# Kernel tuning notes

Measured on AMD Instinct MI355X. Metric: run time of the kernel, lower is better.

Reference implementation:

```python
import jax, jax.numpy as jnp
import numpy as np

N = 8192
D_IN = 1024
D_OUT = 1024


def setup_inputs() -> dict:
    key = jax.random.key(0)
    k0, k1, k2, k3 = jax.random.split(key, 4)
    scale = 1.0 / np.sqrt(D_IN)  # roughly matches nn.Linear init magnitude
    return {
        "x": jax.random.normal(k0, (N, D_IN), dtype=jnp.float32),
        "Wq": jax.random.normal(k1, (D_IN, D_OUT), dtype=jnp.float32) * scale,
        "Wk": jax.random.normal(k2, (D_IN, D_OUT), dtype=jnp.float32) * scale,
        "Wv": jax.random.normal(k3, (D_IN, D_OUT), dtype=jnp.float32) * scale,
    }


def reference(x, Wq, Wk, Wv):
    # QKV projections (bias-free Linear); weights stored [d_in, d_out]
    q = x @ Wq  # [N, d_out]
    k = x @ Wk  # [N, d_out]
    v = x @ Wv  # [N, d_out]
    # full N x N attention scores, scaled by sqrt(d_out), softmax over keys
    scores = jnp.einsum("nd,md->nm", q, k) / jnp.sqrt(jnp.asarray(k.shape[-1], x.dtype))
    weights = jax.nn.softmax(scores, axis=-1)
    return weights @ v  # [N, d_out]
```

## Files before the change

### kernel.cpp

```cpp
#include <hip/hip_runtime.h>
#include <hip/hip_bf16.h>
#include <stdint.h>
#include <stddef.h>

using bf16 = __hip_bfloat16;

typedef __attribute__((ext_vector_type(8))) short bf16x8;
typedef __attribute__((ext_vector_type(4))) float f32x4;

#define NROWS 8192
#define DDIM  1024

#define GLDS16(gsrc, ldst)                                                     \
  __builtin_amdgcn_global_load_lds(                                            \
      (const __attribute__((address_space(1))) uint32_t*)(gsrc),               \
      (__attribute__((address_space(3))) uint32_t*)(ldst), 16, 0, 0)

__global__ void cvt_f32_bf16_k(const float* __restrict__ in, bf16* __restrict__ out, int n) {
  int i = blockIdx.x * blockDim.x + threadIdx.x;
  int idx = i * 4;
  if (idx < n) {
    float4 v = *reinterpret_cast<const float4*>(in + idx);
    alignas(8) bf16 t[4] = {(bf16)v.x, (bf16)v.y, (bf16)v.z, (bf16)v.w};
    *reinterpret_cast<uint2*>(out + idx) = *reinterpret_cast<const uint2*>(t);
  }
}

template <typename Tin>
__global__ void transpose_bf16_k(const Tin* __restrict__ in, bf16* __restrict__ out,
                                 int R, int C) {
  __shared__ float tile[32][33];
  int bx = blockIdx.x * 32;
  int by = blockIdx.y * 32;
  int tx = threadIdx.x, ty = threadIdx.y;
#pragma unroll
  for (int i = 0; i < 32; i += 8)
    tile[ty + i][tx] = (float)in[(size_t)(by + ty + i) * C + (bx + tx)];
  __syncthreads();
#pragma unroll
  for (int i = 0; i < 32; i += 8)
    out[(size_t)(bx + ty + i) * R + (by + tx)] = (bf16)tile[tx][ty + i];
}

__global__ void rowsum_k(const bf16* __restrict__ P, float* __restrict__ Z, int Kc) {
  int lane = threadIdx.x & 63;
  int wave = threadIdx.x >> 6;
  int row = blockIdx.x * 4 + wave;
  const bf16* p = P + (size_t)row * Kc;
  float s = 0.f;
  for (int c = lane * 8; c < Kc; c += 64 * 8) {
    bf16x8 v = *reinterpret_cast<const bf16x8*>(p + c);
#pragma unroll
    for (int j = 0; j < 8; j++)
      s += __uint_as_float(((uint32_t)(uint16_t)v[j]) << 16);
  }
#pragma unroll
  for (int off = 32; off > 0; off >>= 1) s += __shfl_down(s, off);
  if (lane == 0) Z[row] = s;
}

__global__ void combine_k(const float* __restrict__ P0, const float* __restrict__ P1,
                          const float* __restrict__ Z, float* __restrict__ out, int total) {
  int i = blockIdx.x * blockDim.x + threadIdx.x;
  int idx = i * 4;
  if (idx < total) {
    float4 a = *reinterpret_cast<const float4*>(P0 + idx);
    float4 b = *reinterpret_cast<const float4*>(P1 + idx);
    float rz = 1.0f / Z[idx >> 10];
    float4 o;
    o.x = (a.x + b.x) * rz; o.y = (a.y + b.y) * rz;
    o.z = (a.z + b.z) * rz; o.w = (a.w + b.w) * rz;
    *reinterpret_cast<float4*>(out + idx) = o;
  }
}

template <int EPI>
__global__ __launch_bounds__(256) void gemm_bt_k(
    const bf16* __restrict__ A, const bf16* __restrict__ B, void* __restrict__ Cv,
    const float* __restrict__ Z, int M, int N, int K, float scale) {
  __shared__ alignas(16) bf16 As[128 * 32];
  __shared__ alignas(16) bf16 Bs[128 * 32];

  const int tid = threadIdx.x;
  const int lane = tid & 63;
  const int wave = tid >> 6;
  const int wr = (wave >> 1) * 64;
  const int wc = (wave & 1) * 64;

  const int mBase = blockIdx.y * 128;
  const int nBase = blockIdx.x * 128;

  const int srow = tid >> 2;
  const int skel = (tid & 3) * 8;

  const bf16* gA0 = A + (size_t)(mBase + srow) * K + skel;
  const bf16* gA1 = A + (size_t)(mBase + srow + 64) * K + skel;
  const bf16* gB0 = B + (size_t)(nBase + srow) * K + skel;
  const bf16* gB1 = B + (size_t)(nBase + srow + 64) * K + skel;

  bf16* lA0 = &As[srow * 32 + skel];
  bf16* lA1 = &As[(srow + 64) * 32 + skel];
  bf16* lB0 = &Bs[srow * 32 + skel];
  bf16* lB1 = &Bs[(srow + 64) * 32 + skel];

  f32x4 acc[4][4];
  f32x4 zero = {0.f, 0.f, 0.f, 0.f};
#pragma unroll
  for (int i = 0; i < 4; i++)
#pragma unroll
    for (int j = 0; j < 4; j++) acc[i][j] = zero;

  const int fr = lane & 15;
  const int fk = (lane >> 4) * 8;

  for (int k0 = 0; k0 < K; k0 += 32) {
    GLDS16(gA0 + k0, lA0);
    GLDS16(gA1 + k0, lA1);
    GLDS16(gB0 + k0, lB0);
    GLDS16(gB1 + k0, lB1);
    __syncthreads();

    bf16x8 a[4], b[4];
#pragma unroll
    for (int mi = 0; mi < 4; mi++)
      a[mi] = *reinterpret_cast<const bf16x8*>(&As[(wr + mi * 16 + fr) * 32 + fk]);
#pragma unroll
    for (int nj = 0; nj < 4; nj++)
      b[nj] = *reinterpret_cast<const bf16x8*>(&Bs[(wc + nj * 16 + fr) * 32 + fk]);
#pragma unroll
    for (int mi = 0; mi < 4; mi++)
#pragma unroll
      for (int nj = 0; nj < 4; nj++)
        acc[mi][nj] = __builtin_amdgcn_mfma_f32_16x16x32_bf16(a[mi], b[nj], acc[mi][nj], 0, 0, 0);
    __syncthreads();
  }

#pragma unroll
  for (int mi = 0; mi < 4; mi++) {
#pragma unroll
    for (int nj = 0; nj < 4; nj++) {
      int col = nBase + wc + nj * 16 + fr;
#pragma unroll
      for (int j = 0; j < 4; j++) {
        int row = mBase + wr + mi * 16 + (lane >> 4) * 4 + j;
        float v = acc[mi][nj][j];
        if (EPI == 0) {
          ((bf16*)Cv)[(size_t)row * N + col] = (bf16)(v * scale);
        }
      }
    }
  }
}

template <int EPI>
__global__ __launch_bounds__(512, 2) void gemm256_k(
    const bf16* __restrict__ A, const bf16* __restrict__ B, void* __restrict__ Cv,
    int M, int N, int K, int ksplit) {
  __shared__ alignas(1024) bf16 smem[4 * 16384];

  const int tid = threadIdx.x;
  const int lane = tid & 63;
  const int wave = tid >> 6;
  const int wm = wave >> 2;
  const int wn = wave & 3;

  const int nwgx = gridDim.x;
  const int nwg = nwgx * gridDim.y;
  const int wg = blockIdx.y * nwgx + blockIdx.x;
  const int cpx = nwg >> 3;
  const int swz = (wg & 7) * cpx + (wg >> 3);
  const int bx = swz % nwgx;
  const int by = swz / nwgx;
  const int mBase = by * 256;
  const int nBase = bx * 256;

  const int z = blockIdx.z;
  const int kbase = z * ksplit;
  const int NT = ksplit / 32;

  const int sr = lane >> 2;
  const int ssl = (lane & 3) ^ ((lane >> 3) & 3);
  const bf16* srcA0 = A + (size_t)(mBase + wave * 16 + sr) * K + kbase + ssl * 8;
  const bf16* srcA1 = A + (size_t)(mBase + (wave + 8) * 16 + sr) * K + kbase + ssl * 8;
  const bf16* srcB0 = B + (size_t)(nBase + wave * 16 + sr) * K + kbase + ssl * 8;
  const bf16* srcB1 = B + (size_t)(nBase + (wave + 8) * 16 + sr) * K + kbase + ssl * 8;

  const int fr = lane & 15;
  const int laneElem = fr * 32 + (((lane >> 4) ^ ((fr >> 1) & 3)) * 8);

  f32x4 acc[8][4];
  f32x4 zero = {0.f, 0.f, 0.f, 0.f};
#pragma unroll
  for (int m = 0; m < 8; m++)
#pragma unroll
    for (int n = 0; n < 4; n++) acc[m][n] = zero;

  auto stage = [&](int t) {
    bf16* base = smem + (t & 3) * 16384;
    int kk = t * 32;
    GLDS16(srcA0 + kk, base + wave * 512);
    GLDS16(srcA1 + kk, base + (wave + 8) * 512);
    GLDS16(srcB0 + kk, base + 8192 + wave * 512);
    GLDS16(srcB1 + kk, base + 8192 + (wave + 8) * 512);
  };

  stage(0);
  if (NT > 1) stage(1);
  if (NT > 2) stage(2);

  for (int t = 0; t < NT; ++t) {
    __builtin_amdgcn_s_barrier();
    if (t + 3 < NT) stage(t + 3);
    int infl = NT - 1 - t;
    if (infl > 3) infl = 3;
    if (infl == 3)      asm volatile("s_waitcnt vmcnt(12)" ::: "memory");
    else if (infl == 2) asm volatile("s_waitcnt vmcnt(8)" ::: "memory");
    else if (infl == 1) asm volatile("s_waitcnt vmcnt(4)" ::: "memory");
    else                asm volatile("s_waitcnt vmcnt(0)" ::: "memory");
    __builtin_amdgcn_s_barrier();

    const bf16* bufA = smem + (t & 3) * 16384;
    const bf16* bufB = bufA + 8192;
    bf16x8 a[8], b[4];
#pragma unroll
    for (int m = 0; m < 8; m++)
      a[m] = *reinterpret_cast<const bf16x8*>(bufA + (wm * 128 + m * 16) * 32 + laneElem);
#pragma unroll
    for (int n = 0; n < 4; n++)
      b[n] = *reinterpret_cast<const bf16x8*>(bufB + (wn * 64 + n * 16) * 32 + laneElem);
#pragma unroll
    for (int m = 0; m < 8; m++)
#pragma unroll
      for (int n = 0; n < 4; n++)
        acc[m][n] = __builtin_amdgcn_mfma_f32_16x16x32_bf16(a[m], b[n], acc[m][n], 0, 0, 0);
  }

#pragma unroll
  for (int m = 0; m < 8; m++) {
#pragma unroll
    for (int n = 0; n < 4; n++) {
      int col = nBase + wn * 64 + n * 16 + fr;
#pragma unroll
      for (int j = 0; j < 4; j++) {
        int row = mBase + wm * 128 + m * 16 + (lane >> 4) * 4 + j;
        float v = acc[m][n][j];
        if (EPI == 1) {
          ((bf16*)Cv)[(size_t)row * N + col] = (bf16)__expf(v);
        } else {
          float* Cp = (float*)Cv + (size_t)z * M * N;
          Cp[(size_t)row * N + col] = v;
        }
      }
    }
  }
}

extern "C" void kernel_launch(void* const* d_in, const int* in_sizes, int n_in,
                              void* d_out, int out_size, void* d_ws, size_t ws_size,
                              hipStream_t stream) {
  (void)in_sizes; (void)n_in; (void)out_size; (void)ws_size;
  const float* x  = (const float*)d_in[0];
  const float* Wq = (const float*)d_in[1];
  const float* Wk = (const float*)d_in[2];
  const float* Wv = (const float*)d_in[3];
  float* out = (float*)d_out;

  char* ws = (char*)d_ws;
  const size_t MB = 1024 * 1024;
  size_t o = 0;
  float* Z  = (float*)(ws + o); o += 64 * 1024;
  size_t xb_off = o;
  bf16* xb  = (bf16*)(ws + o); o += (size_t)NROWS * DDIM * 2;
  bf16* WqT = (bf16*)(ws + o); o += (size_t)DDIM * DDIM * 2;
  bf16* WkT = (bf16*)(ws + o); o += (size_t)DDIM * DDIM * 2;
  bf16* WvT = (bf16*)(ws + o); o += (size_t)DDIM * DDIM * 2;
  bf16* Qb  = (bf16*)(ws + o); o += (size_t)NROWS * DDIM * 2;
  bf16* Kb  = (bf16*)(ws + o); o += (size_t)NROWS * DDIM * 2;
  bf16* Vb  = (bf16*)(ws + o); o += (size_t)NROWS * DDIM * 2;
  bf16* Vt  = (bf16*)(ws + o); o += (size_t)DDIM * NROWS * 2;
  bf16* P   = (bf16*)(ws + o); o += (size_t)NROWS * NROWS * 2;
  float* Pp = (float*)(ws + xb_off);
  (void)MB;

  {
    int n = NROWS * DDIM;
    cvt_f32_bf16_k<<<(n / 4 + 255) / 256, 256, 0, stream>>>(x, xb, n);
  }
  {
    dim3 tb(32, 8);
    transpose_bf16_k<float><<<dim3(32, 32), tb, 0, stream>>>(Wq, WqT, DDIM, DDIM);
    transpose_bf16_k<float><<<dim3(32, 32), tb, 0, stream>>>(Wk, WkT, DDIM, DDIM);
    transpose_bf16_k<float><<<dim3(32, 32), tb, 0, stream>>>(Wv, WvT, DDIM, DDIM);
  }
  {
    dim3 grid(DDIM / 128, NROWS / 128);
    gemm_bt_k<0><<<grid, 256, 0, stream>>>(xb, WqT, Qb, nullptr, NROWS, DDIM, DDIM, 0.03125f);
    gemm_bt_k<0><<<grid, 256, 0, stream>>>(xb, WkT, Kb, nullptr, NROWS, DDIM, DDIM, 1.0f);
    gemm_bt_k<0><<<grid, 256, 0, stream>>>(xb, WvT, Vb, nullptr, NROWS, DDIM, DDIM, 1.0f);
  }
  {
    dim3 tb(32, 8);
    transpose_bf16_k<bf16><<<dim3(DDIM / 32, NROWS / 32), tb, 0, stream>>>(Vb, Vt, NROWS, DDIM);
  }
  gemm256_k<1><<<dim3(NROWS / 256, NROWS / 256, 1), 512, 0, stream>>>(
      Qb, Kb, P, NROWS, NROWS, DDIM, DDIM);
  rowsum_k<<<NROWS / 4, 256, 0, stream>>>(P, Z, NROWS);
  gemm256_k<3><<<dim3(DDIM / 256, NROWS / 256, 2), 512, 0, stream>>>(
      P, Vt, Pp, NROWS, DDIM, NROWS, NROWS / 2);
  {
    int total = NROWS * DDIM;
    combine_k<<<(total / 4 + 255) / 256, 256, 0, stream>>>(
        Pp, Pp + (size_t)NROWS * DDIM, Z, out, total);
  }
}
```

Measured before the change: 435.3 us.

## Fuse QKV projections, fuse rowsum into exp epilogue, double-buffer LDS fragment reads

Merges the three projection GEMMs into one wide GEMM on the 256-tile kernel, writing an interleaved QKV buffer with stride-aware loads. The softmax row sums are now accumulated in the exp epilogue using shuffles and atomics, so the separate rowsum pass over P is dropped. The main loop is unrolled by two and prefetches the next tile's LDS fragments into registers while MFMAs run, with setprio hints. The trade-offs are atomic contention on Z, higher register pressure, and a memset added to the launch sequence.

```diff
diff --git a/kernel.cpp b/kernel.cpp
--- a/kernel.cpp
+++ b/kernel.cpp
@@ -28,35 +28,18 @@
 
 template <typename Tin>
 __global__ void transpose_bf16_k(const Tin* __restrict__ in, bf16* __restrict__ out,
-                                 int R, int C) {
+                                 int R, int C, int ldin) {
   __shared__ float tile[32][33];
   int bx = blockIdx.x * 32;
   int by = blockIdx.y * 32;
   int tx = threadIdx.x, ty = threadIdx.y;
 #pragma unroll
   for (int i = 0; i < 32; i += 8)
-    tile[ty + i][tx] = (float)in[(size_t)(by + ty + i) * C + (bx + tx)];
+    tile[ty + i][tx] = (float)in[(size_t)(by + ty + i) * ldin + (bx + tx)];
   __syncthreads();
 #pragma unroll
   for (int i = 0; i < 32; i += 8)
     out[(size_t)(bx + ty + i) * R + (by + tx)] = (bf16)tile[tx][ty + i];
-}
-
-__global__ void rowsum_k(const bf16* __restrict__ P, float* __restrict__ Z, int Kc) {
-  int lane = threadIdx.x & 63;
-  int wave = threadIdx.x >> 6;
-  int row = blockIdx.x * 4 + wave;
-  const bf16* p = P + (size_t)row * Kc;
-  float s = 0.f;
-  for (int c = lane * 8; c < Kc; c += 64 * 8) {
-    bf16x8 v = *reinterpret_cast<const bf16x8*>(p + c);
-#pragma unroll
-    for (int j = 0; j < 8; j++)
-      s += __uint_as_float(((uint32_t)(uint16_t)v[j]) << 16);
-  }
-#pragma unroll
-  for (int off = 32; off > 0; off >>= 1) s += __shfl_down(s, off);
-  if (lane == 0) Z[row] = s;
 }
 
 __global__ void combine_k(const float* __restrict__ P0, const float* __restrict__ P1,
@@ -75,87 +58,10 @@
 }
 
 template <int EPI>
-__global__ __launch_bounds__(256) void gemm_bt_k(
-    const bf16* __restrict__ A, const bf16* __restrict__ B, void* __restrict__ Cv,
-    const float* __restrict__ Z, int M, int N, int K, float scale) {
-  __shared__ alignas(16) bf16 As[128 * 32];
-  __shared__ alignas(16) bf16 Bs[128 * 32];
-
-  const int tid = threadIdx.x;
-  const int lane = tid & 63;
-  const int wave = tid >> 6;
-  const int wr = (wave >> 1) * 64;
-  const int wc = (wave & 1) * 64;
-
-  const int mBase = blockIdx.y * 128;
-  const int nBase = blockIdx.x * 128;
-
-  const int srow = tid >> 2;
-  const int skel = (tid & 3) * 8;
-
-  const bf16* gA0 = A + (size_t)(mBase + srow) * K + skel;
-  const bf16* gA1 = A + (size_t)(mBase + srow + 64) * K + skel;
-  const bf16* gB0 = B + (size_t)(nBase + srow) * K + skel;
-  const bf16* gB1 = B + (size_t)(nBase + srow + 64) * K + skel;
-
-  bf16* lA0 = &As[srow * 32 + skel];
-  bf16* lA1 = &As[(srow + 64) * 32 + skel];
-  bf16* lB0 = &Bs[srow * 32 + skel];
-  bf16* lB1 = &Bs[(srow + 64) * 32 + skel];
-
-  f32x4 acc[4][4];
-  f32x4 zero = {0.f, 0.f, 0.f, 0.f};
-#pragma unroll
-  for (int i = 0; i < 4; i++)
-#pragma unroll
-    for (int j = 0; j < 4; j++) acc[i][j] = zero;
-
-  const int fr = lane & 15;
-  const int fk = (lane >> 4) * 8;
-
-  for (int k0 = 0; k0 < K; k0 += 32) {
-    GLDS16(gA0 + k0, lA0);
-    GLDS16(gA1 + k0, lA1);
-    GLDS16(gB0 + k0, lB0);
-    GLDS16(gB1 + k0, lB1);
-    __syncthreads();
-
-    bf16x8 a[4], b[4];
-#pragma unroll
-    for (int mi = 0; mi < 4; mi++)
-      a[mi] = *reinterpret_cast<const bf16x8*>(&As[(wr + mi * 16 + fr) * 32 + fk]);
-#pragma unroll
-    for (int nj = 0; nj < 4; nj++)
-      b[nj] = *reinterpret_cast<const bf16x8*>(&Bs[(wc + nj * 16 + fr) * 32 + fk]);
-#pragma unroll
-    for (int mi = 0; mi < 4; mi++)
-#pragma unroll
-      for (int nj = 0; nj < 4; nj++)
-        acc[mi][nj] = __builtin_amdgcn_mfma_f32_16x16x32_bf16(a[mi], b[nj], acc[mi][nj], 0, 0, 0);
-    __syncthreads();
-  }
-
-#pragma unroll
-  for (int mi = 0; mi < 4; mi++) {
-#pragma unroll
-    for (int nj = 0; nj < 4; nj++) {
-      int col = nBase + wc + nj * 16 + fr;
-#pragma unroll
-      for (int j = 0; j < 4; j++) {
-        int row = mBase + wr + mi * 16 + (lane >> 4) * 4 + j;
-        float v = acc[mi][nj][j];
-        if (EPI == 0) {
-          ((bf16*)Cv)[(size_t)row * N + col] = (bf16)(v * scale);
-        }
-      }
-    }
-  }
-}
-
-template <int EPI>
 __global__ __launch_bounds__(512, 2) void gemm256_k(
     const bf16* __restrict__ A, const bf16* __restrict__ B, void* __restrict__ Cv,
-    int M, int N, int K, int ksplit) {
+    float* __restrict__ Zp, int M, int N, int K, int lda, int ldb, int ldc,
+    int ksplit, float scale) {
   __shared__ alignas(1024) bf16 smem[4 * 16384];
 
   const int tid = threadIdx.x;
@@ -180,10 +86,10 @@
 
   const int sr = lane >> 2;
   const int ssl = (lane & 3) ^ ((lane >> 3) & 3);
-  const bf16* srcA0 = A + (size_t)(mBase + wave * 16 + sr) * K + kbase + ssl * 8;
-  const bf16* srcA1 = A + (size_t)(mBase + (wave + 8) * 16 + sr) * K + kbase + ssl * 8;
-  const bf16* srcB0 = B + (size_t)(nBase + wave * 16 + sr) * K + kbase + ssl * 8;
-  const bf16* srcB1 = B + (size_t)(nBase + (wave + 8) * 16 + sr) * K + kbase + ssl * 8;
+  const bf16* srcA0 = A + (size_t)(mBase + wave * 16 + sr) * lda + kbase + ssl * 8;
+  const bf16* srcA1 = A + (size_t)(mBase + (wave + 8) * 16 + sr) * lda + kbase + ssl * 8;
+  const bf16* srcB0 = B + (size_t)(nBase + wave * 16 + sr) * ldb + kbase + ssl * 8;
+  const bf16* srcB1 = B + (size_t)(nBase + (wave + 8) * 16 + sr) * ldb + kbase + ssl * 8;
 
   const int fr = lane & 15;
   const int laneElem = fr * 32 + (((lane >> 4) ^ ((fr >> 1) & 3)) * 8);
@@ -203,36 +109,80 @@
     GLDS16(srcB0 + kk, base + 8192 + wave * 512);
     GLDS16(srcB1 + kk, base + 8192 + (wave + 8) * 512);
   };
+  auto rdA = [&](const bf16* buf, int m) {
+    return *reinterpret_cast<const bf16x8*>(buf + wm * 4096 + m * 512 + laneElem);
+  };
+  auto rdB = [&](const bf16* buf, int n) {
+    return *reinterpret_cast<const bf16x8*>(buf + 8192 + wn * 2048 + n * 512 + laneElem);
+  };
+
+  bf16x8 fA0[8], fB0[4], fA1[8], fB1[4];
+
+  auto compute = [&](int t, bf16x8 (&aC)[8], bf16x8 (&bC)[4],
+                     bf16x8 (&aN)[8], bf16x8 (&bN)[4], bool rd) {
+    const bf16* nb = smem + ((t + 1) & 3) * 16384;
+#pragma unroll
+    for (int c = 0; c < 4; c++) {
+      if (rd) {
+        aN[2 * c]     = rdA(nb, 2 * c);
+        aN[2 * c + 1] = rdA(nb, 2 * c + 1);
+        bN[c]         = rdB(nb, c);
+      }
+      __builtin_amdgcn_s_setprio(1);
+#pragma unroll
+      for (int mm = 0; mm < 2; mm++)
+#pragma unroll
+        for (int n = 0; n < 4; n++)
+          acc[2 * c + mm][n] = __builtin_amdgcn_mfma_f32_16x16x32_bf16(
+              aC[2 * c + mm], bC[n], acc[2 * c + mm][n], 0, 0, 0);
+      __builtin_amdgcn_s_setprio(0);
+    }
+  };
 
   stage(0);
-  if (NT > 1) stage(1);
-  if (NT > 2) stage(2);
-
-  for (int t = 0; t < NT; ++t) {
-    __builtin_amdgcn_s_barrier();
-    if (t + 3 < NT) stage(t + 3);
-    int infl = NT - 1 - t;
-    if (infl > 3) infl = 3;
-    if (infl == 3)      asm volatile("s_waitcnt vmcnt(12)" ::: "memory");
-    else if (infl == 2) asm volatile("s_waitcnt vmcnt(8)" ::: "memory");
-    else if (infl == 1) asm volatile("s_waitcnt vmcnt(4)" ::: "memory");
-    else                asm volatile("s_waitcnt vmcnt(0)" ::: "memory");
-    __builtin_amdgcn_s_barrier();
-
-    const bf16* bufA = smem + (t & 3) * 16384;
-    const bf16* bufB = bufA + 8192;
-    bf16x8 a[8], b[4];
+  stage(1);
+  stage(2);
+  asm volatile("s_waitcnt vmcnt(8)" ::: "memory");
+  __builtin_amdgcn_s_barrier();
+#pragma unroll
+  for (int m = 0; m < 8; m++) fA0[m] = rdA(smem, m);
+#pragma unroll
+  for (int n = 0; n < 4; n++) fB0[n] = rdB(smem, n);
+
+#define WAITV(infl)                                                            \
+  do {                                                                         \
+    if ((infl) >= 2)      asm volatile("s_waitcnt vmcnt(8)" ::: "memory");     \
+    else if ((infl) == 1) asm volatile("s_waitcnt vmcnt(4)" ::: "memory");     \
+    else                  asm volatile("s_waitcnt vmcnt(0)" ::: "memory");     \
+  } while (0)
+
+  for (int u = 0; u < NT; u += 2) {
+    __builtin_amdgcn_s_barrier();
+    if (u + 3 < NT) stage(u + 3);
+    {
+      int hi = (u + 3 < NT - 1) ? (u + 3) : (NT - 1);
+      WAITV(hi - (u + 1));
+    }
+    __builtin_amdgcn_s_barrier();
+    compute(u, fA0, fB0, fA1, fB1, true);
+
+    __builtin_amdgcn_s_barrier();
+    if (u + 4 < NT) stage(u + 4);
+    if (u + 2 < NT) {
+      int hi = (u + 4 < NT - 1) ? (u + 4) : (NT - 1);
+      WAITV(hi - (u + 2));
+    }
+    __builtin_amdgcn_s_barrier();
+    compute(u + 1, fA1, fB1, fA0, fB0, (u + 2 < NT));
+  }
+#undef WAITV
+
+  float rs[8][4];
+  if (EPI == 1) {
 #pragma unroll
     for (int m = 0; m < 8; m++)
-      a[m] = *reinterpret_cast<const bf16x8*>(bufA + (wm * 128 + m * 16) * 32 + laneElem);
-#pragma unroll
-    for (int n = 0; n < 4; n++)
-      b[n] = *reinterpret_cast<const bf16x8*>(bufB + (wn * 64 + n * 16) * 32 + laneElem);
-#pragma unroll
-    for (int m = 0; m < 8; m++)
-#pragma unroll
-      for (int n = 0; n < 4; n++)
-        acc[m][n] = __builtin_amdgcn_mfma_f32_16x16x32_bf16(a[m], b[n], acc[m][n], 0, 0, 0);
+#pragma unroll
+      for (int j = 0; j < 4; j++) rs[m][j] = 0.f;
   }
 
 #pragma unroll
@@ -244,11 +194,33 @@
       for (int j = 0; j < 4; j++) {
         int row = mBase + wm * 128 + m * 16 + (lane >> 4) * 4 + j;
         float v = acc[m][n][j];
-        if (EPI == 1) {
-          ((bf16*)Cv)[(size_t)row * N + col] = (bf16)__expf(v);
+        if (EPI == 0) {
+          ((bf16*)Cv)[(size_t)row * ldc + col] = (bf16)v;
+        } else if (EPI == 1) {
+          float ev = __expf(v * scale);
+          rs[m][j] += ev;
+          ((bf16*)Cv)[(size_t)row * ldc + col] = (bf16)ev;
         } else {
-          float* Cp = (float*)Cv + (size_t)z * M * N;
-          Cp[(size_t)row * N + col] = v;
+          float* Cp = (float*)Cv + (size_t)z * M * ldc;
+          Cp[(size_t)row * ldc + col] = v;
+        }
+      }
+    }
+  }
+
+  if (EPI == 1) {
+#pragma unroll
+    for (int m = 0; m < 8; m++) {
+#pragma unroll
+      for (int j = 0; j < 4; j++) {
+        float s = rs[m][j];
+        s += __shfl_xor(s, 1);
+        s += __shfl_xor(s, 2);
+        s += __shfl_xor(s, 4);
+        s += __shfl_xor(s, 8);
+        if (fr == 0) {
+          int row = mBase + wm * 128 + m * 16 + (lane >> 4) * 4 + j;
+          atomicAdd(&Zp[row], s);
         }
       }
     }
@@ -266,47 +238,42 @@
   float* out = (float*)d_out;
 
   char* ws = (char*)d_ws;
-  const size_t MB = 1024 * 1024;
   size_t o = 0;
-  float* Z  = (float*)(ws + o); o += 64 * 1024;
+  float* Z   = (float*)(ws + o); o += 64 * 1024;
   size_t xb_off = o;
-  bf16* xb  = (bf16*)(ws + o); o += (size_t)NROWS * DDIM * 2;
-  bf16* WqT = (bf16*)(ws + o); o += (size_t)DDIM * DDIM * 2;
-  bf16* WkT = (bf16*)(ws + o); o += (size_t)DDIM * DDIM * 2;
-  bf16* WvT = (bf16*)(ws + o); o += (size_t)DDIM * DDIM * 2;
-  bf16* Qb  = (bf16*)(ws + o); o += (size_t)NROWS * DDIM * 2;
-  bf16* Kb  = (bf16*)(ws + o); o += (size_t)NROWS * DDIM * 2;
-  bf16* Vb  = (bf16*)(ws + o); o += (size_t)NROWS * DDIM * 2;
-  bf16* Vt  = (bf16*)(ws + o); o += (size_t)DDIM * NROWS * 2;
-  bf16* P   = (bf16*)(ws + o); o += (size_t)NROWS * NROWS * 2;
-  float* Pp = (float*)(ws + xb_off);
-  (void)MB;
-
+  bf16* xb    = (bf16*)(ws + o); o += (size_t)NROWS * DDIM * 2;
+  bf16* WqkvT = (bf16*)(ws + o); o += (size_t)3 * DDIM * DDIM * 2;
+  bf16* QKV   = (bf16*)(ws + o); o += (size_t)NROWS * 3 * DDIM * 2;
+  bf16* Vt    = (bf16*)(ws + o); o += (size_t)DDIM * NROWS * 2;
+  bf16* P     = (bf16*)(ws + o); o += (size_t)NROWS * NROWS * 2;
+  float* Pp   = (float*)(ws + xb_off);
+
+  bf16* Qb = QKV;
+  bf16* Kb = QKV + DDIM;
+  bf16* Vb = QKV + 2 * DDIM;
+
+  hipMemsetAsync(Z, 0, NROWS * sizeof(float), stream);
   {
     int n = NROWS * DDIM;
     cvt_f32_bf16_k<<<(n / 4 + 255) / 256, 256, 0, stream>>>(x, xb, n);
   }
   {
     dim3 tb(32, 8);
-    transpose_bf16_k<float><<<dim3(32, 32), tb, 0, stream>>>(Wq, WqT, DDIM, DDIM);
-    transpose_bf16_k<float><<<dim3(32, 32), tb, 0, stream>>>(Wk, WkT, DDIM, DDIM);
-    transpose_bf16_k<float><<<dim3(32, 32), tb, 0, stream>>>(Wv, WvT, DDIM, DDIM);
-  }
-  {
-    dim3 grid(DDIM / 128, NROWS / 128);
-    gemm_bt_k<0><<<grid, 256, 0, stream>>>(xb, WqT, Qb, nullptr, NROWS, DDIM, DDIM, 0.03125f);
-    gemm_bt_k<0><<<grid, 256, 0, stream>>>(xb, WkT, Kb, nullptr, NROWS, DDIM, DDIM, 1.0f);
-    gemm_bt_k<0><<<grid, 256, 0, stream>>>(xb, WvT, Vb, nullptr, NROWS, DDIM, DDIM, 1.0f);
-  }
+    transpose_bf16_k<float><<<dim3(32, 32), tb, 0, stream>>>(Wq, WqkvT,                DDIM, DDIM, DDIM);
+    transpose_bf16_k<float><<<dim3(32, 32), tb, 0, stream>>>(Wk, WqkvT + 1024 * 1024,  DDIM, DDIM, DDIM);
+    transpose_bf16_k<float><<<dim3(32, 32), tb, 0, stream>>>(Wv, WqkvT + 2048 * 1024,  DDIM, DDIM, DDIM);
+  }
+  gemm256_k<0><<<dim3(3 * DDIM / 256, NROWS / 256, 1), 512, 0, stream>>>(
+      xb, WqkvT, QKV, nullptr, NROWS, 3 * DDIM, DDIM, DDIM, DDIM, 3 * DDIM, DDIM, 1.0f);
   {
     dim3 tb(32, 8);
-    transpose_bf16_k<bf16><<<dim3(DDIM / 32, NROWS / 32), tb, 0, stream>>>(Vb, Vt, NROWS, DDIM);
+    transpose_bf16_k<bf16><<<dim3(DDIM / 32, NROWS / 32), tb, 0, stream>>>(
+        Vb, Vt, NROWS, DDIM, 3 * DDIM);
   }
   gemm256_k<1><<<dim3(NROWS / 256, NROWS / 256, 1), 512, 0, stream>>>(
-      Qb, Kb, P, NROWS, NROWS, DDIM, DDIM);
-  rowsum_k<<<NROWS / 4, 256, 0, stream>>>(P, Z, NROWS);
+      Qb, Kb, P, Z, NROWS, NROWS, DDIM, 3 * DDIM, 3 * DDIM, NROWS, DDIM, 0.03125f);
   gemm256_k<3><<<dim3(DDIM / 256, NROWS / 256, 2), 512, 0, stream>>>(
-      P, Vt, Pp, NROWS, DDIM, NROWS, NROWS / 2);
+      P, Vt, Pp, nullptr, NROWS, DDIM, NROWS, NROWS, NROWS, DDIM, NROWS / 2, 1.0f);
   {
     int total = NROWS * DDIM;
     combine_k<<<(total / 4 + 255) / 256, 256, 0, stream>>>(
```

After: 457.2 us. +5.0%, slower.
